# Optimization experiments

Hardware: AMD Instinct MI355X
Metric: run time of the kernel (lower is better)

The kernel has to match this reference:

```python
import jax, jax.numpy as jnp
import numpy as np

N_ITER = 50  # default n_iter of entmax.entmax_bisect


def entmax_bisect(X, alpha, n_iter=N_ITER):
    """alpha-entmax over the last axis via bisection (entmax package algorithm)."""
    d = X.shape[-1]
    am1 = alpha - 1.0
    inv = 1.0 / am1
    Xa = X * am1

    def p(z):  # clamp(z,0)**(1/(alpha-1)), grad-safe at 0
        return jnp.where(z > 0, jnp.maximum(z, 1e-30) ** inv, 0.0)

    max_val = jnp.max(Xa, axis=-1, keepdims=True)
    tau_lo = max_val - 1.0                       # _gp(1, alpha) = 1
    tau_hi = max_val - (1.0 / d) ** am1          # _gp(1/d, alpha)
    f_lo = jnp.sum(p(Xa - tau_lo), axis=-1, keepdims=True) - 1.0
    dm0 = tau_hi - tau_lo

    def body(carry, _):
        tau_lo, dm, _ = carry
        dm = dm * 0.5
        tau_m = tau_lo + dm
        f_m = jnp.sum(p(Xa - tau_m), axis=-1, keepdims=True) - 1.0
        tau_lo = jnp.where(f_m * f_lo >= 0, tau_m, tau_lo)
        return (tau_lo, dm, tau_m), None

    (_, _, tau_m), _ = jax.lax.scan(body, (tau_lo, dm0, tau_lo), None, length=n_iter)
    pm = p(Xa - tau_m)
    return pm / jnp.sum(pm, axis=-1, keepdims=True)  # ensure_sum_one=True


def setup_inputs() -> dict:
    key = jax.random.key(0)
    ks = jax.random.split(key, 10)
    b, c, e, h = 8, 2048, 64, 8
    s_in = 1.0 / np.sqrt(e)
    s_u = 1.0 / np.sqrt(h * e)
    x = jax.random.normal(ks[0], (b, c, e), jnp.float32)
    Wk = jax.random.normal(ks[1], (h * e, e), jnp.float32) * s_in
    bk = jax.random.normal(ks[2], (h * e,), jnp.float32) * 0.01
    Wq = jax.random.normal(ks[3], (h * e, e), jnp.float32) * s_in
    bq = jax.random.normal(ks[4], (h * e,), jnp.float32) * 0.01
    Wv = jax.random.normal(ks[5], (h * e, e), jnp.float32) * s_in
    bv = jax.random.normal(ks[6], (h * e,), jnp.float32) * 0.01
    Wu = jax.random.normal(ks[7], (e, h * e), jnp.float32) * s_u
    bu = jax.random.normal(ks[8], (e,), jnp.float32) * 0.01
    alpha = jnp.asarray(1.5, jnp.float32)  # learned scalar
    return dict(x=x, alpha=alpha, Wk=Wk, bk=bk, Wq=Wq, bq=bq,
                Wv=Wv, bv=bv, Wu=Wu, bu=bu)


def reference(x, alpha, Wk, bk, Wq, bq, Wv, bv, Wu, bu):
    b, c, e = x.shape
    h = Wk.shape[0] // e
    k = (x @ Wk.T + bk).reshape(b, c, h, e)
    q = (x @ Wq.T + bq).reshape(b, c, h, e)
    v = (x @ Wv.T + bv).reshape(b, c, h, e)
    # dot[b,c,i,j] = sum_h q[b,c,h,i] * k[b,c,h,j] / sqrt(e)   (per-token e x e scores)
    dot = jnp.einsum('bchi,bchj->bcij', q, k) / np.sqrt(e).astype(np.float32)
    att = entmax_bisect(dot, alpha)
    # res[b,c,h,i] = sum_j att[b,c,i,j] * v[b,c,h,j]
    res = jnp.einsum('bcij,bchj->bchi', att, v).reshape(b, c, h * e)
    return res @ Wu.T + bu
```

## Files before the change

kernel.cpp:

```cpp
#include <hip/hip_runtime.h>
#include <math.h>

#define NTOK 16384
#define EDIM 64
#define HHE  512
#define TOKPAD 260

typedef _Float16 half8 __attribute__((ext_vector_type(8)));
typedef __fp16   half2v __attribute__((ext_vector_type(2)));
typedef float    floatx4 __attribute__((ext_vector_type(4)));

__device__ __forceinline__ half8 cvt8(const float4 a, const float4 b) {
    half8 h;
    h[0] = (_Float16)a.x; h[1] = (_Float16)a.y;
    h[2] = (_Float16)a.z; h[3] = (_Float16)a.w;
    h[4] = (_Float16)b.x; h[5] = (_Float16)b.y;
    h[6] = (_Float16)b.z; h[7] = (_Float16)b.w;
    return h;
}

__device__ __forceinline__ float dot2(half2v a, half2v b, float c) {
#if __has_builtin(__builtin_amdgcn_fdot2)
    return __builtin_amdgcn_fdot2(a, b, c, false);
#else
    return fmaf((float)a[0], (float)b[0], fmaf((float)a[1], (float)b[1], c));
#endif
}
__device__ __forceinline__ half2v pk(float x, float y) {
    return __builtin_amdgcn_cvt_pkrtz(x, y);
}
union h2u { half2v h; unsigned int u; };

__device__ __forceinline__ float clamp01(float z) {
    return __builtin_amdgcn_fmed3f(z, 0.0f, 1.0f);
}
__device__ __forceinline__ float pgen(float z, float inv) {
    return z > 0.0f ? exp2f(inv * log2f(fmaxf(z, 1e-30f))) : 0.0f;
}

__global__ __launch_bounds__(256) void cvt_fp16_kernel(
    const float* __restrict__ x,
    const float* __restrict__ Wk, const float* __restrict__ Wq,
    const float* __restrict__ Wv, const float* __restrict__ Wu,
    __fp16* __restrict__ xh, __fp16* __restrict__ wkh,
    __fp16* __restrict__ wqh, __fp16* __restrict__ wvh,
    __fp16* __restrict__ wuh)
{
    const int z = blockIdx.y;
    const float* src; __fp16* dst; int n;
    if      (z == 0) { src = x;  dst = xh;  n = NTOK * EDIM; }
    else if (z == 1) { src = Wk; dst = wkh; n = HHE * EDIM; }
    else if (z == 2) { src = Wq; dst = wqh; n = HHE * EDIM; }
    else if (z == 3) { src = Wv; dst = wvh; n = HHE * EDIM; }
    else             { src = Wu; dst = wuh; n = EDIM * HHE; }
    const int idx = (blockIdx.x * 256 + threadIdx.x) * 8;
    if (idx < n) {
        const float4 a = *(const float4*)(src + idx);
        const float4 b = *(const float4*)(src + idx + 4);
        *(half8*)(dst + idx) = cvt8(a, b);
    }
}

__global__ __launch_bounds__(256) void qkv_attn_out_kernel(
    const __fp16* __restrict__ xh,
    const __fp16* __restrict__ wkh, const float* __restrict__ bk,
    const __fp16* __restrict__ wqh, const float* __restrict__ bq,
    const __fp16* __restrict__ wvh, const float* __restrict__ bv,
    const __fp16* __restrict__ wuh, const float* __restrict__ bu,
    float* __restrict__ out, const float* alpha_p)
{
    __shared__ __align__(16) half2v qT[16 * TOKPAD];
    __shared__ __align__(16) half2v kT[16 * TOKPAD];
    __shared__ __align__(16) half2v vT[16 * TOKPAD];

    const int tid  = threadIdx.x;
    const int lane = tid & 63;
    const int w    = tid >> 6;
    const int tok0 = blockIdx.x * 16;

    const int m    = lane & 15;
    const int quad = lane >> 4;

    const __fp16* xrow = xh + (size_t)(tok0 + m) * EDIM + quad * 8;
    half8 bfr[2];
    bfr[0] = *(const half8*)(xrow);
    bfr[1] = *(const half8*)(xrow + 32);

    #pragma unroll
    for (int uu = 0; uu < 3; ++uu) {
        const int unit = w * 3 + uu;
        const int z    = unit >> 2;
        const int col0 = (unit & 3) * 128;
        const __fp16* W   = (z == 0) ? wkh : (z == 1) ? wqh : wvh;
        const float* bias = (z == 0) ? bk : (z == 1) ? bq : bv;
        half2v* dstT      = (z == 0) ? kT : (z == 1) ? qT : vT;

        #pragma unroll
        for (int ct = 0; ct < 8; ++ct) {
            const int n = col0 + ct * 16 + m;
            const int grow = (z < 2) ? ((n & 7) * 64 + (n >> 3)) : n;
            const __fp16* wrow = W + (size_t)grow * EDIM + quad * 8;
            floatx4 acc = (floatx4){0.f, 0.f, 0.f, 0.f};
            #pragma unroll
            for (int kc = 0; kc < 2; ++kc) {
                const half8 af = *(const half8*)(wrow + kc * 32);
                acc = __builtin_amdgcn_mfma_f32_16x16x32_f16(af, bfr[kc], acc, 0, 0, 0);
            }
            h2u p0, p1;
            if (z < 2) {
                const int hbase = 4 * (quad & 1);
                const int j     = (col0 >> 3) + ct * 2 + (quad >> 1);
                float o0 = acc[0] + bias[(hbase + 0) * 64 + j];
                float o1 = acc[1] + bias[(hbase + 1) * 64 + j];
                float o2 = acc[2] + bias[(hbase + 2) * 64 + j];
                float o3 = acc[3] + bias[(hbase + 3) * 64 + j];
                p0.h = pk(o0, o1);
                p1.h = pk(o2, o3);
                uint2 st; st.x = p0.u; st.y = p1.u;
                *(uint2*)&dstT[m * TOKPAD + j * 4 + 2 * (quad & 1)] = st;
            } else {
                const int nn = col0 + ct * 16 + quad * 4;
                const int h  = nn >> 6;
                const int jj = nn & 63;
                const float4 b4 = *(const float4*)&bias[nn];
                p0.h = pk(acc[0] + b4.x, acc[1] + b4.y);
                p1.h = pk(acc[2] + b4.z, acc[3] + b4.w);
                uint2 st; st.x = p0.u; st.y = p1.u;
                *(uint2*)&dstT[m * TOKPAD + h * 32 + (jj >> 1)] = st;
            }
        }
    }
    __syncthreads();

    const float alpha = alpha_p[0];
    const float am1   = alpha - 1.0f;
    __fp16* resL = (__fp16*)qT;

    for (int i = 0; i < 4; ++i) {
        const int t = w * 4 + i;

        union { half8 h8; half2v h2[4]; } uq;
        uq.h8 = *(const half8*)&qT[t * TOKPAD + lane * 4];

        float row[64];
        #pragma unroll
        for (int j = 0; j < 64; ++j) {
            union { half8 h8; half2v h2[4]; } u;
            u.h8 = *(const half8*)&kT[t * TOKPAD + j * 4];
            float d = dot2(uq.h2[0], u.h2[0], 0.0f);
            d = dot2(uq.h2[1], u.h2[1], d);
            d = dot2(uq.h2[2], u.h2[2], d);
            d = dot2(uq.h2[3], u.h2[3], d);
            row[j] = d;
        }

        const float scale = am1 * 0.125f;
        #pragma unroll
        for (int j = 0; j < 64; ++j) row[j] *= scale;

        float mx = row[0];
        #pragma unroll
        for (int j = 1; j < 64; ++j) mx = fmaxf(mx, row[j]);

        float tau_lo = mx - 1.0f;
        const float tau_hi = mx - exp2f(-6.0f * am1);
        float dm = tau_hi - tau_lo;
        float inv_sum;

        if (am1 == 0.5f) {
            #pragma unroll
            for (int it = 0; it < 6; ++it) {
                dm *= 0.5f;
                const float tau_m = tau_lo + dm;
                float f0 = -1.0f, f1 = 0.0f, f2 = 0.0f, f3 = 0.0f;
                #pragma unroll
                for (int j = 0; j < 64; j += 4) {
                    const float a0 = clamp01(row[j+0] - tau_m);
                    const float a1 = clamp01(row[j+1] - tau_m);
                    const float a2 = clamp01(row[j+2] - tau_m);
                    const float a3 = clamp01(row[j+3] - tau_m);
                    f0 = fmaf(a0, a0, f0); f1 = fmaf(a1, a1, f1);
                    f2 = fmaf(a2, a2, f2); f3 = fmaf(a3, a3, f3);
                }
                const float f = (f0 + f1) + (f2 + f3);
                tau_lo = (f >= 0.0f) ? tau_m : tau_lo;
            }
            float tau = tau_lo;
            #pragma unroll
            for (int it = 0; it < 2; ++it) {
                float f0 = -1.0f, f1 = 0.0f, f2 = 0.0f, f3 = 0.0f;
                float s0 = 0.0f, s1 = 0.0f, s2 = 0.0f, s3 = 0.0f;
                #pragma unroll
                for (int j = 0; j < 64; j += 4) {
                    const float a0 = clamp01(row[j+0] - tau);
                    const float a1 = clamp01(row[j+1] - tau);
                    const float a2 = clamp01(row[j+2] - tau);
                    const float a3 = clamp01(row[j+3] - tau);
                    f0 = fmaf(a0, a0, f0); f1 = fmaf(a1, a1, f1);
                    f2 = fmaf(a2, a2, f2); f3 = fmaf(a3, a3, f3);
                    s0 += a0; s1 += a1; s2 += a2; s3 += a3;
                }
                const float f = (f0 + f1) + (f2 + f3);
                const float s = ((s0 + s1) + (s2 + s3)) + 1e-20f;
                tau = tau + fmaxf(f, 0.0f) / (s + s);
            }
            float s0 = 0.0f, s1 = 0.0f;
            #pragma unroll
            for (int j = 0; j < 64; j += 2) {
                float a0 = clamp01(row[j+0] - tau);
                float a1 = clamp01(row[j+1] - tau);
                a0 *= a0; a1 *= a1;
                row[j+0] = a0; row[j+1] = a1;
                s0 += a0; s1 += a1;
            }
            inv_sum = 1.0f / (s0 + s1);
        } else {
            const float inv = 1.0f / am1;
            float tau_m = tau_lo;
            float f_lo = -1.0f;
            #pragma unroll
            for (int j = 0; j < 64; ++j) f_lo += pgen(row[j] - tau_lo, inv);
            for (int it = 0; it < 30; ++it) {
                dm *= 0.5f;
                tau_m = tau_lo + dm;
                float f = -1.0f;
                #pragma unroll
                for (int j = 0; j < 64; ++j) f += pgen(row[j] - tau_m, inv);
                tau_lo = (f * f_lo >= 0.0f) ? tau_m : tau_lo;
            }
            float s = 0.0f;
            #pragma unroll
            for (int j = 0; j < 64; ++j) {
                const float pm = pgen(row[j] - tau_m, inv);
                row[j] = pm;
                s += pm;
            }
            inv_sum = 1.0f / s;
        }

        half2v p2[32];
        #pragma unroll
        for (int ii = 0; ii < 32; ++ii) p2[ii] = pk(row[2 * ii], row[2 * ii + 1]);

        float acc[8];
        #pragma unroll
        for (int h = 0; h < 8; ++h) {
            float a0 = 0.0f, a1 = 0.0f;
            #pragma unroll
            for (int jc = 0; jc < 8; ++jc) {
                union { half8 h8; half2v h2[4]; } u;
                u.h8 = *(const half8*)&vT[t * TOKPAD + h * 32 + jc * 4];
                a0 = dot2(p2[jc * 4 + 0], u.h2[0], a0);
                a1 = dot2(p2[jc * 4 + 1], u.h2[1], a1);
                a0 = dot2(p2[jc * 4 + 2], u.h2[2], a0);
                a1 = dot2(p2[jc * 4 + 3], u.h2[3], a1);
            }
            acc[h] = a0 + a1;
        }
        #pragma unroll
        for (int h = 0; h < 8; ++h)
            resL[t * 520 + h * 64 + lane] = (__fp16)(acc[h] * inv_sum);
    }
    __syncthreads();

    {
        floatx4 oacc = (floatx4){0.f, 0.f, 0.f, 0.f};
        const __fp16* rrow = resL + (size_t)m * 520 + quad * 8;
        const __fp16* wrow = wuh + (size_t)(w * 16 + m) * HHE + quad * 8;
        #pragma unroll
        for (int kc = 0; kc < 16; ++kc) {
            const half8 bf = *(const half8*)(rrow + kc * 32);
            const half8 af = *(const half8*)(wrow + kc * 32);
            oacc = __builtin_amdgcn_mfma_f32_16x16x32_f16(af, bf, oacc, 0, 0, 0);
        }
        const int tok = tok0 + m;
        const int col = w * 16 + quad * 4;
        const float4 b4 = *(const float4*)&bu[col];
        float4 o;
        o.x = oacc[0] + b4.x;
        o.y = oacc[1] + b4.y;
        o.z = oacc[2] + b4.z;
        o.w = oacc[3] + b4.w;
        *(float4*)&out[(size_t)tok * 64 + col] = o;
    }
}

extern "C" void kernel_launch(void* const* d_in, const int* in_sizes, int n_in,
                              void* d_out, int out_size, void* d_ws, size_t ws_size,
                              hipStream_t stream)
{
    const float* x     = (const float*)d_in[0];
    const float* alpha = (const float*)d_in[1];
    const float* Wk    = (const float*)d_in[2];
    const float* bk    = (const float*)d_in[3];
    const float* Wq    = (const float*)d_in[4];
    const float* bq    = (const float*)d_in[5];
    const float* Wv    = (const float*)d_in[6];
    const float* bv    = (const float*)d_in[7];
    const float* Wu    = (const float*)d_in[8];
    const float* bu    = (const float*)d_in[9];
    float* out = (float*)d_out;

    __fp16* xh   = (__fp16*)d_ws;
    __fp16* wkh  = xh  + (size_t)NTOK * EDIM;
    __fp16* wqh  = wkh + (size_t)HHE * EDIM;
    __fp16* wvh  = wqh + (size_t)HHE * EDIM;
    __fp16* wuh  = wvh + (size_t)HHE * EDIM;

    cvt_fp16_kernel<<<dim3(512, 5), 256, 0, stream>>>(
        x, Wk, Wq, Wv, Wu, xh, wkh, wqh, wvh, wuh);
    qkv_attn_out_kernel<<<NTOK / 16, 256, 0, stream>>>(
        xh, wkh, bk, wqh, bq, wvh, bv, wuh, bu, out, alpha);
}
```

Measured before the change: 158.2 us.

## Fold x conversion into main kernel, prescale Wq, use packed f32 math in entmax

Removes the separate fp16 conversion pass over x and converts x in registers inside the fused kernel, so the conversion kernel only handles the small weights. The (alpha-1)/8 score scale is folded into Wq and bq, which removes a per-element multiply. The entmax bisection and Newton loops switch to v_pk_add/v_pk_fma/v_pk_mul on float pairs, drop the upper clamp, and pack probabilities straight to fp16. It also adds a fast reciprocal. The risk is extra fp16 rounding from pre-scaling Wq, plus inline asm that limits compiler scheduling.

```diff
diff --git a/kernel.cpp b/kernel.cpp
--- a/kernel.cpp
+++ b/kernel.cpp
@@ -9,6 +9,7 @@
 typedef _Float16 half8 __attribute__((ext_vector_type(8)));
 typedef __fp16   half2v __attribute__((ext_vector_type(2)));
 typedef float    floatx4 __attribute__((ext_vector_type(4)));
+typedef float    float2v __attribute__((ext_vector_type(2)));
 
 __device__ __forceinline__ half8 cvt8(const float4 a, const float4 b) {
     half8 h;
@@ -31,38 +32,50 @@
 }
 union h2u { half2v h; unsigned int u; };
 
-__device__ __forceinline__ float clamp01(float z) {
-    return __builtin_amdgcn_fmed3f(z, 0.0f, 1.0f);
-}
+__device__ __forceinline__ float2v pk_add(float2v a, float2v b) {
+    float2v d;
+    asm("v_pk_add_f32 %0, %1, %2" : "=v"(d) : "v"(a), "v"(b));
+    return d;
+}
+__device__ __forceinline__ float2v pk_mul(float2v a, float2v b) {
+    float2v d;
+    asm("v_pk_mul_f32 %0, %1, %2" : "=v"(d) : "v"(a), "v"(b));
+    return d;
+}
+__device__ __forceinline__ float2v pk_fma(float2v a, float2v b, float2v c) {
+    float2v d;
+    asm("v_pk_fma_f32 %0, %1, %2, %3" : "=v"(d) : "v"(a), "v"(b), "v"(c));
+    return d;
+}
+
 __device__ __forceinline__ float pgen(float z, float inv) {
     return z > 0.0f ? exp2f(inv * log2f(fmaxf(z, 1e-30f))) : 0.0f;
 }
 
 __global__ __launch_bounds__(256) void cvt_fp16_kernel(
-    const float* __restrict__ x,
     const float* __restrict__ Wk, const float* __restrict__ Wq,
     const float* __restrict__ Wv, const float* __restrict__ Wu,
-    __fp16* __restrict__ xh, __fp16* __restrict__ wkh,
-    __fp16* __restrict__ wqh, __fp16* __restrict__ wvh,
-    __fp16* __restrict__ wuh)
+    __fp16* __restrict__ wkh, __fp16* __restrict__ wqh,
+    __fp16* __restrict__ wvh, __fp16* __restrict__ wuh,
+    const float* alpha_p)
 {
     const int z = blockIdx.y;
-    const float* src; __fp16* dst; int n;
-    if      (z == 0) { src = x;  dst = xh;  n = NTOK * EDIM; }
-    else if (z == 1) { src = Wk; dst = wkh; n = HHE * EDIM; }
-    else if (z == 2) { src = Wq; dst = wqh; n = HHE * EDIM; }
-    else if (z == 3) { src = Wv; dst = wvh; n = HHE * EDIM; }
-    else             { src = Wu; dst = wuh; n = EDIM * HHE; }
+    const float* src; __fp16* dst;
+    float s = 1.0f;
+    if      (z == 0) { src = Wk; dst = wkh; }
+    else if (z == 1) { src = Wq; dst = wqh; s = (alpha_p[0] - 1.0f) * 0.125f; }
+    else if (z == 2) { src = Wv; dst = wvh; }
+    else             { src = Wu; dst = wuh; }
     const int idx = (blockIdx.x * 256 + threadIdx.x) * 8;
-    if (idx < n) {
-        const float4 a = *(const float4*)(src + idx);
-        const float4 b = *(const float4*)(src + idx + 4);
-        *(half8*)(dst + idx) = cvt8(a, b);
-    }
+    float4 a = *(const float4*)(src + idx);
+    float4 b = *(const float4*)(src + idx + 4);
+    a.x *= s; a.y *= s; a.z *= s; a.w *= s;
+    b.x *= s; b.y *= s; b.z *= s; b.w *= s;
+    *(half8*)(dst + idx) = cvt8(a, b);
 }
 
 __global__ __launch_bounds__(256) void qkv_attn_out_kernel(
-    const __fp16* __restrict__ xh,
+    const float* __restrict__ x,
     const __fp16* __restrict__ wkh, const float* __restrict__ bk,
     const __fp16* __restrict__ wqh, const float* __restrict__ bq,
     const __fp16* __restrict__ wvh, const float* __restrict__ bv,
@@ -81,10 +94,20 @@
     const int m    = lane & 15;
     const int quad = lane >> 4;
 
-    const __fp16* xrow = xh + (size_t)(tok0 + m) * EDIM + quad * 8;
+    const float alpha = alpha_p[0];
+    const float am1   = alpha - 1.0f;
+    const float s_q   = am1 * 0.125f;
+
+    const float* xrow = x + (size_t)(tok0 + m) * EDIM + quad * 8;
     half8 bfr[2];
-    bfr[0] = *(const half8*)(xrow);
-    bfr[1] = *(const half8*)(xrow + 32);
+    {
+        const float4 a0 = *(const float4*)(xrow);
+        const float4 a1 = *(const float4*)(xrow + 4);
+        const float4 a2 = *(const float4*)(xrow + 32);
+        const float4 a3 = *(const float4*)(xrow + 36);
+        bfr[0] = cvt8(a0, a1);
+        bfr[1] = cvt8(a2, a3);
+    }
 
     #pragma unroll
     for (int uu = 0; uu < 3; ++uu) {
@@ -94,6 +117,7 @@
         const __fp16* W   = (z == 0) ? wkh : (z == 1) ? wqh : wvh;
         const float* bias = (z == 0) ? bk : (z == 1) ? bq : bv;
         half2v* dstT      = (z == 0) ? kT : (z == 1) ? qT : vT;
+        const float bs    = (z == 1) ? s_q : 1.0f;
 
         #pragma unroll
         for (int ct = 0; ct < 8; ++ct) {
@@ -110,10 +134,10 @@
             if (z < 2) {
                 const int hbase = 4 * (quad & 1);
                 const int j     = (col0 >> 3) + ct * 2 + (quad >> 1);
-                float o0 = acc[0] + bias[(hbase + 0) * 64 + j];
-                float o1 = acc[1] + bias[(hbase + 1) * 64 + j];
-                float o2 = acc[2] + bias[(hbase + 2) * 64 + j];
-                float o3 = acc[3] + bias[(hbase + 3) * 64 + j];
+                float o0 = fmaf(bias[(hbase + 0) * 64 + j], bs, acc[0]);
+                float o1 = fmaf(bias[(hbase + 1) * 64 + j], bs, acc[1]);
+                float o2 = fmaf(bias[(hbase + 2) * 64 + j], bs, acc[2]);
+                float o3 = fmaf(bias[(hbase + 3) * 64 + j], bs, acc[3]);
                 p0.h = pk(o0, o1);
                 p1.h = pk(o2, o3);
                 uint2 st; st.x = p0.u; st.y = p1.u;
@@ -132,8 +156,6 @@
     }
     __syncthreads();
 
-    const float alpha = alpha_p[0];
-    const float am1   = alpha - 1.0f;
     __fp16* resL = (__fp16*)qT;
 
     for (int i = 0; i < 4; ++i) {
@@ -142,105 +164,139 @@
         union { half8 h8; half2v h2[4]; } uq;
         uq.h8 = *(const half8*)&qT[t * TOKPAD + lane * 4];
 
-        float row[64];
-        #pragma unroll
-        for (int j = 0; j < 64; ++j) {
-            union { half8 h8; half2v h2[4]; } u;
-            u.h8 = *(const half8*)&kT[t * TOKPAD + j * 4];
-            float d = dot2(uq.h2[0], u.h2[0], 0.0f);
-            d = dot2(uq.h2[1], u.h2[1], d);
-            d = dot2(uq.h2[2], u.h2[2], d);
-            d = dot2(uq.h2[3], u.h2[3], d);
-            row[j] = d;
-        }
-
-        const float scale = am1 * 0.125f;
-        #pragma unroll
-        for (int j = 0; j < 64; ++j) row[j] *= scale;
-
-        float mx = row[0];
-        #pragma unroll
-        for (int j = 1; j < 64; ++j) mx = fmaxf(mx, row[j]);
+        float2v rowv[32];
+        #pragma unroll
+        for (int j = 0; j < 64; j += 2) {
+            union { half8 h8; half2v h2[4]; } u0, u1;
+            u0.h8 = *(const half8*)&kT[t * TOKPAD + j * 4];
+            u1.h8 = *(const half8*)&kT[t * TOKPAD + (j + 1) * 4];
+            float d0 = dot2(uq.h2[0], u0.h2[0], 0.0f);
+            float d1 = dot2(uq.h2[0], u1.h2[0], 0.0f);
+            d0 = dot2(uq.h2[1], u0.h2[1], d0);
+            d1 = dot2(uq.h2[1], u1.h2[1], d1);
+            d0 = dot2(uq.h2[2], u0.h2[2], d0);
+            d1 = dot2(uq.h2[2], u1.h2[2], d1);
+            d0 = dot2(uq.h2[3], u0.h2[3], d0);
+            d1 = dot2(uq.h2[3], u1.h2[3], d1);
+            rowv[j >> 1] = (float2v){d0, d1};
+        }
+
+        float m0 = fmaxf(rowv[0].x, rowv[0].y);
+        float m1 = fmaxf(rowv[1].x, rowv[1].y);
+        float m2 = fmaxf(rowv[2].x, rowv[2].y);
+        float m3 = fmaxf(rowv[3].x, rowv[3].y);
+        #pragma unroll
+        for (int jj = 4; jj < 32; jj += 4) {
+            m0 = fmaxf(m0, fmaxf(rowv[jj + 0].x, rowv[jj + 0].y));
+            m1 = fmaxf(m1, fmaxf(rowv[jj + 1].x, rowv[jj + 1].y));
+            m2 = fmaxf(m2, fmaxf(rowv[jj + 2].x, rowv[jj + 2].y));
+            m3 = fmaxf(m3, fmaxf(rowv[jj + 3].x, rowv[jj + 3].y));
+        }
+        const float mx = fmaxf(fmaxf(m0, m1), fmaxf(m2, m3));
 
         float tau_lo = mx - 1.0f;
         const float tau_hi = mx - exp2f(-6.0f * am1);
         float dm = tau_hi - tau_lo;
         float inv_sum;
+        half2v p2[32];
 
         if (am1 == 0.5f) {
             #pragma unroll
             for (int it = 0; it < 6; ++it) {
                 dm *= 0.5f;
                 const float tau_m = tau_lo + dm;
-                float f0 = -1.0f, f1 = 0.0f, f2 = 0.0f, f3 = 0.0f;
+                const float2v nt = {-tau_m, -tau_m};
+                float2v f0 = {-1.0f, 0.0f}, f1 = {0.0f, 0.0f},
+                        f2 = {0.0f, 0.0f}, f3 = {0.0f, 0.0f};
                 #pragma unroll
-                for (int j = 0; j < 64; j += 4) {
-                    const float a0 = clamp01(row[j+0] - tau_m);
-                    const float a1 = clamp01(row[j+1] - tau_m);
-                    const float a2 = clamp01(row[j+2] - tau_m);
-                    const float a3 = clamp01(row[j+3] - tau_m);
-                    f0 = fmaf(a0, a0, f0); f1 = fmaf(a1, a1, f1);
-                    f2 = fmaf(a2, a2, f2); f3 = fmaf(a3, a3, f3);
+                for (int jj = 0; jj < 32; jj += 4) {
+                    float2v a0 = pk_add(rowv[jj + 0], nt);
+                    float2v a1 = pk_add(rowv[jj + 1], nt);
+                    float2v a2 = pk_add(rowv[jj + 2], nt);
+                    float2v a3 = pk_add(rowv[jj + 3], nt);
+                    a0.x = fmaxf(a0.x, 0.0f); a0.y = fmaxf(a0.y, 0.0f);
+                    a1.x = fmaxf(a1.x, 0.0f); a1.y = fmaxf(a1.y, 0.0f);
+                    a2.x = fmaxf(a2.x, 0.0f); a2.y = fmaxf(a2.y, 0.0f);
+                    a3.x = fmaxf(a3.x, 0.0f); a3.y = fmaxf(a3.y, 0.0f);
+                    f0 = pk_fma(a0, a0, f0);
+                    f1 = pk_fma(a1, a1, f1);
+                    f2 = pk_fma(a2, a2, f2);
+                    f3 = pk_fma(a3, a3, f3);
                 }
-                const float f = (f0 + f1) + (f2 + f3);
+                const float2v ft = pk_add(pk_add(f0, f1), pk_add(f2, f3));
+                const float f = ft.x + ft.y;
                 tau_lo = (f >= 0.0f) ? tau_m : tau_lo;
             }
             float tau = tau_lo;
             #pragma unroll
             for (int it = 0; it < 2; ++it) {
-                float f0 = -1.0f, f1 = 0.0f, f2 = 0.0f, f3 = 0.0f;
-                float s0 = 0.0f, s1 = 0.0f, s2 = 0.0f, s3 = 0.0f;
+                const float2v nt = {-tau, -tau};
+                float2v f0 = {-1.0f, 0.0f}, f1 = {0.0f, 0.0f};
+                float2v s0 = {0.0f, 0.0f}, s1 = {0.0f, 0.0f};
                 #pragma unroll
-                for (int j = 0; j < 64; j += 4) {
-                    const float a0 = clamp01(row[j+0] - tau);
-                    const float a1 = clamp01(row[j+1] - tau);
-                    const float a2 = clamp01(row[j+2] - tau);
-                    const float a3 = clamp01(row[j+3] - tau);
-                    f0 = fmaf(a0, a0, f0); f1 = fmaf(a1, a1, f1);
-                    f2 = fmaf(a2, a2, f2); f3 = fmaf(a3, a3, f3);
-                    s0 += a0; s1 += a1; s2 += a2; s3 += a3;
+                for (int jj = 0; jj < 32; jj += 2) {
+                    float2v a0 = pk_add(rowv[jj + 0], nt);
+                    float2v a1 = pk_add(rowv[jj + 1], nt);
+                    a0.x = fmaxf(a0.x, 0.0f); a0.y = fmaxf(a0.y, 0.0f);
+                    a1.x = fmaxf(a1.x, 0.0f); a1.y = fmaxf(a1.y, 0.0f);
+                    f0 = pk_fma(a0, a0, f0);
+                    f1 = pk_fma(a1, a1, f1);
+                    s0 = pk_add(s0, a0);
+                    s1 = pk_add(s1, a1);
                 }
-                const float f = (f0 + f1) + (f2 + f3);
-                const float s = ((s0 + s1) + (s2 + s3)) + 1e-20f;
-                tau = tau + fmaxf(f, 0.0f) / (s + s);
-            }
-            float s0 = 0.0f, s1 = 0.0f;
-            #pragma unroll
-            for (int j = 0; j < 64; j += 2) {
-                float a0 = clamp01(row[j+0] - tau);
-                float a1 = clamp01(row[j+1] - tau);
-                a0 *= a0; a1 *= a1;
-                row[j+0] = a0; row[j+1] = a1;
-                s0 += a0; s1 += a1;
-            }
-            inv_sum = 1.0f / (s0 + s1);
+                const float2v ft = pk_add(f0, f1);
+                const float2v st = pk_add(s0, s1);
+                const float f = ft.x + ft.y;
+                const float s = (st.x + st.y) + 1e-20f;
+                tau = tau + fmaxf(f, 0.0f) * __builtin_amdgcn_rcpf(s + s);
+            }
+            const float2v nt = {-tau, -tau};
+            float2v sa = {0.0f, 0.0f}, sb = {0.0f, 0.0f};
+            #pragma unroll
+            for (int jj = 0; jj < 32; jj += 2) {
+                float2v a0 = pk_add(rowv[jj + 0], nt);
+                float2v a1 = pk_add(rowv[jj + 1], nt);
+                a0.x = fmaxf(a0.x, 0.0f); a0.y = fmaxf(a0.y, 0.0f);
+                a1.x = fmaxf(a1.x, 0.0f); a1.y = fmaxf(a1.y, 0.0f);
+                const float2v q0 = pk_mul(a0, a0);
+                const float2v q1 = pk_mul(a1, a1);
+                sa = pk_add(sa, q0);
+                sb = pk_add(sb, q1);
+                p2[jj + 0] = pk(q0.x, q0.y);
+                p2[jj + 1] = pk(q1.x, q1.y);
+            }
+            const float2v st = pk_add(sa, sb);
+            inv_sum = 1.0f / (st.x + st.y);
         } else {
             const float inv = 1.0f / am1;
             float tau_m = tau_lo;
             float f_lo = -1.0f;
             #pragma unroll
-            for (int j = 0; j < 64; ++j) f_lo += pgen(row[j] - tau_lo, inv);
+            for (int jj = 0; jj < 32; ++jj) {
+                f_lo += pgen(rowv[jj].x - tau_lo, inv);
+                f_lo += pgen(rowv[jj].y - tau_lo, inv);
+            }
             for (int it = 0; it < 30; ++it) {
                 dm *= 0.5f;
                 tau_m = tau_lo + dm;
                 float f = -1.0f;
                 #pragma unroll
-                for (int j = 0; j < 64; ++j) f += pgen(row[j] - tau_m, inv);
+                for (int jj = 0; jj < 32; ++jj) {
+                    f += pgen(rowv[jj].x - tau_m, inv);
+                    f += pgen(rowv[jj].y - tau_m, inv);
+                }
                 tau_lo = (f * f_lo >= 0.0f) ? tau_m : tau_lo;
             }
             float s = 0.0f;
             #pragma unroll
-            for (int j = 0; j < 64; ++j) {
-                const float pm = pgen(row[j] - tau_m, inv);
-                row[j] = pm;
-                s += pm;
+            for (int jj = 0; jj < 32; ++jj) {
+                const float pa = pgen(rowv[jj].x - tau_m, inv);
+                const float pb = pgen(rowv[jj].y - tau_m, inv);
+                p2[jj] = pk(pa, pb);
+                s += pa + pb;
             }
             inv_sum = 1.0f / s;
         }
-
-        half2v p2[32];
-        #pragma unroll
-        for (int ii = 0; ii < 32; ++ii) p2[ii] = pk(row[2 * ii], row[2 * ii + 1]);
 
         float acc[8];
         #pragma unroll
@@ -301,14 +357,13 @@
     const float* bu    = (const float*)d_in[9];
     float* out = (float*)d_out;
 
-    __fp16* xh   = (__fp16*)d_ws;
-    __fp16* wkh  = xh  + (size_t)NTOK * EDIM;
+    __fp16* wkh  = (__fp16*)d_ws;
     __fp16* wqh  = wkh + (size_t)HHE * EDIM;
     __fp16* wvh  = wqh + (size_t)HHE * EDIM;
     __fp16* wuh  = wvh + (size_t)HHE * EDIM;
 
-    cvt_fp16_kernel<<<dim3(512, 5), 256, 0, stream>>>(
-        x, Wk, Wq, Wv, Wu, xh, wkh, wqh, wvh, wuh);
+    cvt_fp16_kernel<<<dim3(16, 4), 256, 0, stream>>>(
+        Wk, Wq, Wv, Wu, wkh, wqh, wvh, wuh, alpha);
     qkv_attn_out_kernel<<<NTOK / 16, 256, 0, stream>>>(
-        xh, wkh, bk, wqh, bq, wvh, bv, wuh, bu, out, alpha);
-}
+        x, wkh, bk, wqh, bq, wvh, bv, wuh, bu, out, alpha);
+}
```

Measured after the change: 177.0 us. 11.9% more time.
